# Kernel optimization log

Measured on AMD Instinct MI355X. Metric: run time of the kernel, lower is better.

Reference implementation:

```python
import jax, jax.numpy as jnp
import numpy as np
jax.config.update('jax_enable_x64', True)

T = 524288      # hash table size (2^19)
D = 3           # input_dim
F = 2           # feature_dim
L = 16          # levels
N_MIN, N_MAX = 16, 512
B = 262144      # batch of query points
V = 2 ** D      # voxel corners

_b = np.exp((np.log(N_MAX) - np.log(N_MIN)) / (L - 1))
RESOLUTIONS = jnp.asarray(np.floor(N_MIN * _b ** np.arange(L)).astype(np.int64)).reshape(1, 1, L, 1)
PRIMES = jnp.asarray(np.array([1, 2654435761, 805459861], dtype=np.int64))
_border = np.empty((D, V), dtype=np.int64)
for i in range(D):
    _border[i, :] = np.array(([0] * 2 ** i + [1] * 2 ** i) * 2 ** (D - i - 1), dtype=np.int64)
BORDER_ADDS = jnp.asarray(_border).reshape(1, D, 1, V)


def setup_inputs() -> dict:
    key = jax.random.key(0)
    kx, kt = jax.random.split(key)
    x = jax.random.uniform(kx, (B, D), dtype=jnp.float32)  # coords in [0,1)
    # nn.Embedding init: uniform(-1e-4, 1e-4) per level
    tables = jax.random.uniform(kt, (L, T, F), dtype=jnp.float32, minval=-1e-4, maxval=1e-4)
    return {"x": x, "tables": tables}


def reference(x, tables):
    # scale to each grid resolution: (B, D, L, 1)
    scaled = x[:, :, None, None] * RESOLUTIONS.astype(x.dtype)
    # voxel corner integer coords: (B, D, L, V)
    grid = jnp.floor(scaled).astype(jnp.int64) + BORDER_ADDS
    # NVIDIA fast hash: xor of coord*prime over dims, mod T -> (B, L, V)
    hashed = grid * PRIMES.reshape(1, D, 1, 1)
    idx = jnp.remainder(jnp.bitwise_xor(jnp.bitwise_xor(hashed[:, 0], hashed[:, 1]), hashed[:, 2]), T)
    # gather per-level features: (B, L, V, F)
    feats = tables[jnp.arange(L)[None, :, None], idx]
    # multilinear interpolation weights: prod over dims -> (B, L, V)
    w = jnp.prod(1.0 - jnp.abs(scaled - grid.astype(scaled.dtype)), axis=1)
    # weighted corner sum -> (B, L, F) -> (B, L*F)
    out = jnp.einsum('blv,blvf->blf', w, feats)
    return out.reshape(x.shape[0], L * F)
```

## Files before the change

### kernel.cpp

```cpp
#include <hip/hip_runtime.h>


constexpr int      kT      = 524288;
constexpr unsigned kMask   = kT - 1;
constexpr int      kB      = 262144;
constexpr unsigned kP1     = 2654435761u;
constexpr unsigned kP2     = 805459861u;
constexpr int      kBins   = 4096;
constexpr int      kCap    = 128;
constexpr int      kOvfCap = 65536;
constexpr int      kCoopTot = 845;

typedef float f32x4 __attribute__((ext_vector_type(4)));
typedef float f32x2 __attribute__((ext_vector_type(2)));

__device__ __forceinline__ unsigned morton12(float x0, float x1, float x2) {
    unsigned a = min(15u, (unsigned)(x0 * 16.0f));
    unsigned b = min(15u, (unsigned)(x1 * 16.0f));
    unsigned c = min(15u, (unsigned)(x2 * 16.0f));
    unsigned key = 0;
#pragma unroll
    for (int i = 3; i >= 0; --i)
        key = (key << 3) | (((a >> i) & 1u) << 2) | (((b >> i) & 1u) << 1) | ((c >> i) & 1u);
    return key;
}

__device__ __forceinline__ f32x2 direct_level(const float x0, const float x1, const float x2,
                                              const float res,
                                              const f32x4* __restrict__ tab4) {
    const float s0 = x0 * res, s1 = x1 * res, s2 = x2 * res;
    const float f0 = floorf(s0), f1 = floorf(s1), f2 = floorf(s2);
    const float r0 = s0 - f0, r1 = s1 - f1, r2 = s2 - f2;
    const unsigned c0 = (unsigned)f0;
    const unsigned h1a = (unsigned)f1 * kP1, h1b = h1a + kP1;
    const unsigned h2a = (unsigned)f2 * kP2, h2b = h2a + kP2;
    const float w0a = 1.0f - r0, w1a = 1.0f - r1, w2a = 1.0f - r2;
    float a0 = 0.0f, a1 = 0.0f;
#pragma unroll
    for (int q = 0; q < 4; ++q) {
        const unsigned g = ((q & 1) ? h1b : h1a) ^ ((q & 2) ? h2b : h2a);
        const unsigned i0 = (c0 ^ g) & kMask;
        const unsigned i1 = ((c0 + 1u) ^ g) & kMask;
        const f32x4 A = tab4[i0 >> 1];
        const f32x4 B = tab4[i1 >> 1];
        const float p0x = (i0 & 1) ? A.z : A.x;
        const float p0y = (i0 & 1) ? A.w : A.y;
        const float p1x = (i1 & 1) ? B.z : B.x;
        const float p1y = (i1 & 1) ? B.w : B.y;
        const float wyz = ((q & 1) ? r1 : w1a) * ((q & 2) ? r2 : w2a);
        const float wl = wyz * w0a;
        const float wr = wyz * r0;
        a0 = fmaf(wl, p0x, fmaf(wr, p1x, a0));
        a1 = fmaf(wl, p0y, fmaf(wr, p1y, a1));
    }
    f32x2 r; r.x = a0; r.y = a1;
    return r;
}

__device__ __forceinline__ f32x2 direct_level_masked(const float x0, const float x1, const float x2,
                                                     const float res,
                                                     const f32x4* __restrict__ tab4) {
    const float s0 = x0 * res, s1 = x1 * res, s2 = x2 * res;
    const float f0 = floorf(s0), f1 = floorf(s1), f2 = floorf(s2);
    const float r0 = s0 - f0, r1 = s1 - f1, r2 = s2 - f2;
    const unsigned c0 = (unsigned)f0;
    const unsigned h1a = (unsigned)f1 * kP1, h1b = h1a + kP1;
    const unsigned h2a = (unsigned)f2 * kP2, h2b = h2a + kP2;
    const float w0a = 1.0f - r0, w1a = 1.0f - r1, w2a = 1.0f - r2;

    unsigned i0[4], i1[4];
#pragma unroll
    for (int q = 0; q < 4; ++q) {
        const unsigned g = ((q & 1) ? h1b : h1a) ^ ((q & 2) ? h2b : h2a);
        i0[q] = (c0 ^ g) & kMask;
        i1[q] = ((c0 + 1u) ^ g) & kMask;
    }
    f32x4 A[4];
#pragma unroll
    for (int q = 0; q < 4; ++q) A[q] = tab4[i0[q] >> 1];
    const bool odd = (c0 & 1u) != 0u;
    f32x4 Bv[4];
    if (odd) {
#pragma unroll
        for (int q = 0; q < 4; ++q) Bv[q] = tab4[i1[q] >> 1];
    }
    float a0 = 0.0f, a1 = 0.0f;
#pragma unroll
    for (int q = 0; q < 4; ++q) {
        const float p0x = (i0[q] & 1) ? A[q].z : A[q].x;
        const float p0y = (i0[q] & 1) ? A[q].w : A[q].y;
        const float ex = (i1[q] & 1) ? A[q].z : A[q].x;
        const float ey = (i1[q] & 1) ? A[q].w : A[q].y;
        const float bx_ = (i1[q] & 1) ? Bv[q].z : Bv[q].x;
        const float by_ = (i1[q] & 1) ? Bv[q].w : Bv[q].y;
        const float p1x = odd ? bx_ : ex;
        const float p1y = odd ? by_ : ey;
        const float wyz = ((q & 1) ? r1 : w1a) * ((q & 2) ? r2 : w2a);
        const float wl = wyz * w0a;
        const float wr = wyz * r0;
        a0 = fmaf(wl, p0x, fmaf(wr, p1x, a0));
        a1 = fmaf(wl, p0y, fmaf(wr, p1y, a1));
    }
    f32x2 r; r.x = a0; r.y = a1;
    return r;
}

__device__ __forceinline__ void hashenc_body(const float x0, const float x1, const float x2,
                                             const f32x4* __restrict__ tab4base,
                                             f32x4* __restrict__ out, const unsigned sid) {
    f32x4 o[8];
    constexpr float kResF[16] = {16, 20, 25, 32, 40, 50, 64, 80,
                                 101, 128, 161, 203, 256, 322, 406, 512};
#pragma unroll
    for (int l = 0; l < 16; ++l) {
        const f32x2 r = direct_level(x0, x1, x2, kResF[l], tab4base + (size_t)l * (kT / 2));
        if (l & 1) { o[l >> 1].z = r.x; o[l >> 1].w = r.y; }
        else       { o[l >> 1].x = r.x; o[l >> 1].y = r.y; }
    }
    f32x4* op = out + (size_t)sid * 8;
#pragma unroll
    for (int k = 0; k < 8; ++k) __builtin_nontemporal_store(o[k], op + k);
}

template <int L, int N, int RES, int OFF>
__device__ __forceinline__ void coop_fill(const unsigned lane,
                                          const unsigned bx, const unsigned by, const unsigned bz,
                                          const f32x2* __restrict__ tab2,
                                          f32x2* __restrict__ wlds) {
    const unsigned lo0 = (bx * RES) >> 4, lo1 = (by * RES) >> 4, lo2 = (bz * RES) >> 4;
    const unsigned h1 = lo1 * kP1, h2 = lo2 * kP2;
    constexpr int NC = N * N * N;
#pragma unroll
    for (int k = 0; k < (NC + 63) / 64; ++k) {
        const int t = (int)lane + 64 * k;
        if (t < NC) {
            const unsigned dx = (unsigned)t / (N * N);
            const unsigned rem = (unsigned)t % (N * N);
            const unsigned dy = rem / N, dz = rem % N;
            const unsigned idx = ((lo0 + dx) ^ (h1 + dy * kP1) ^ (h2 + dz * kP2)) & kMask;
            wlds[OFF + t] = tab2[(size_t)L * kT + idx];
        }
    }
}

template <int N, int RES, int OFF>
__device__ __forceinline__ f32x2 coop_interp(const float x0, const float x1, const float x2,
                                             const unsigned bx, const unsigned by, const unsigned bz,
                                             const f32x2* __restrict__ wlds) {
    const float res = (float)RES;
    const float s0 = x0 * res, s1 = x1 * res, s2 = x2 * res;
    const float f0 = floorf(s0), f1 = floorf(s1), f2 = floorf(s2);
    const float r0 = s0 - f0, r1 = s1 - f1, r2 = s2 - f2;
    const unsigned lo0 = (bx * RES) >> 4, lo1 = (by * RES) >> 4, lo2 = (bz * RES) >> 4;
    const unsigned i0 = min((unsigned)f0 - lo0, (unsigned)(N - 2));
    const unsigned i1 = min((unsigned)f1 - lo1, (unsigned)(N - 2));
    const unsigned i2 = min((unsigned)f2 - lo2, (unsigned)(N - 2));
    const int s00 = OFF + (int)(i0 * (N * N) + i1 * N + i2);
    const f32x2 c000 = wlds[s00],             c001 = wlds[s00 + 1];
    const f32x2 c010 = wlds[s00 + N],         c011 = wlds[s00 + N + 1];
    const f32x2 c100 = wlds[s00 + N * N],     c101 = wlds[s00 + N * N + 1];
    const f32x2 c110 = wlds[s00 + N * N + N], c111 = wlds[s00 + N * N + N + 1];
    const float w0a = 1.f - r0, w1a = 1.f - r1, w2a = 1.f - r2;
    const float w00 = w0a * w1a, w01 = w0a * r1, w10 = r0 * w1a, w11 = r0 * r1;
    float a0 = w00 * w2a * c000.x;
    float a1 = w00 * w2a * c000.y;
    a0 = fmaf(w00 * r2,  c001.x, a0); a1 = fmaf(w00 * r2,  c001.y, a1);
    a0 = fmaf(w01 * w2a, c010.x, a0); a1 = fmaf(w01 * w2a, c010.y, a1);
    a0 = fmaf(w01 * r2,  c011.x, a0); a1 = fmaf(w01 * r2,  c011.y, a1);
    a0 = fmaf(w10 * w2a, c100.x, a0); a1 = fmaf(w10 * w2a, c100.y, a1);
    a0 = fmaf(w10 * r2,  c101.x, a0); a1 = fmaf(w10 * r2,  c101.y, a1);
    a0 = fmaf(w11 * w2a, c110.x, a0); a1 = fmaf(w11 * w2a, c110.y, a1);
    a0 = fmaf(w11 * r2,  c111.x, a0); a1 = fmaf(w11 * r2,  c111.y, a1);
    f32x2 r; r.x = a0; r.y = a1;
    return r;
}

__global__ __launch_bounds__(256) void scatter_kernel(const float* __restrict__ x,
                                                      unsigned* __restrict__ cnt,
                                                      f32x4* __restrict__ xsort,
                                                      f32x4* __restrict__ ovf) {
    const int i = blockIdx.x * 256 + threadIdx.x;
    const float x0 = x[3 * i], x1 = x[3 * i + 1], x2 = x[3 * i + 2];
    const unsigned key = morton12(x0, x1, x2);
    const unsigned slot = atomicAdd(&cnt[key], 1u);
    f32x4 v;
    v.x = x0; v.y = x1; v.z = x2; v.w = __uint_as_float((unsigned)i);
    if (slot < (unsigned)kCap) {
        xsort[key * kCap + slot] = v;
    } else {
        const unsigned o = atomicAdd(&cnt[kBins], 1u);
        if (o < (unsigned)kOvfCap) ovf[o] = v;
    }
}

__global__ __launch_bounds__(256, 5) void hashenc_main(const float* __restrict__ x,
                                                       const f32x4* __restrict__ xsort,
                                                       const unsigned* __restrict__ cnt,
                                                       const f32x2* __restrict__ tab2,
                                                       const f32x4* __restrict__ tab4base,
                                                       f32x4* __restrict__ out) {
    __shared__ f32x2 lds[4][kCoopTot];
    const int tid = threadIdx.x;
    const int b = (int)blockIdx.x;

    if (b < 2048) {
        constexpr float kFineRes[8] = {101, 128, 161, 203, 256, 322, 406, 512};
        const int j = b & 7;
        const int chunk = b >> 3;
        const float res = kFineRes[j];
        const f32x4* __restrict__ tab4 = tab4base + (size_t)(8 + j) * (kT / 2);
        f32x2* __restrict__ out2 = (f32x2*)out;
        const int sbase = chunk * 1024 + tid;
#pragma unroll
        for (int it = 0; it < 4; ++it) {
            const int s = sbase + 256 * it;
            const float x0 = x[3 * s + 0];
            const float x1 = x[3 * s + 1];
            const float x2 = x[3 * s + 2];
            const f32x2 r = direct_level_masked(x0, x1, x2, res, tab4);
            __builtin_nontemporal_store(r, out2 + (size_t)s * 16 + 8 + j);
        }
        return;
    }

    const int c = b - 2048;
    const int bid = (int)((c & 7) * 256 + (c >> 3));
    const int gs  = bid * 256 + tid;
    const int bin = gs >> 7;
    const int sl  = gs & (kCap - 1);
    const unsigned n = min(cnt[bin], (unsigned)kCap);
    if ((unsigned)(sl & 64) >= n) return;
    const bool valid = (unsigned)sl < n;
    const f32x4 v = xsort[gs];
    const float x0 = valid ? v.x : 0.5f;
    const float x1 = valid ? v.y : 0.5f;
    const float x2 = valid ? v.z : 0.5f;

    const unsigned key = (unsigned)bin;
    const unsigned bx = ((key >> 2) & 1) | ((key >> 4) & 2) | ((key >> 6) & 4) | ((key >> 8) & 8);
    const unsigned by = ((key >> 1) & 1) | ((key >> 3) & 2) | ((key >> 5) & 4) | ((key >> 7) & 8);
    const unsigned bz = ((key     ) & 1) | ((key >> 2) & 2) | ((key >> 4) & 4) | ((key >> 6) & 8);

    f32x2* wlds = lds[tid >> 6];
    const unsigned lane = (unsigned)(tid & 63);

    coop_fill<0, 2, 16,   0>(lane, bx, by, bz, tab2, wlds);
    coop_fill<1, 4, 20,   8>(lane, bx, by, bz, tab2, wlds);
    coop_fill<2, 4, 25,  72>(lane, bx, by, bz, tab2, wlds);
    coop_fill<3, 3, 32, 136>(lane, bx, by, bz, tab2, wlds);
    coop_fill<4, 5, 40, 163>(lane, bx, by, bz, tab2, wlds);
    coop_fill<5, 6, 50, 288>(lane, bx, by, bz, tab2, wlds);
    coop_fill<6, 5, 64, 504>(lane, bx, by, bz, tab2, wlds);
    coop_fill<7, 6, 80, 629>(lane, bx, by, bz, tab2, wlds);

    f32x4 o0, o1, o2, o3;
    { const f32x2 r = coop_interp<2, 16,   0>(x0, x1, x2, bx, by, bz, wlds); o0.x = r.x; o0.y = r.y; }
    { const f32x2 r = coop_interp<4, 20,   8>(x0, x1, x2, bx, by, bz, wlds); o0.z = r.x; o0.w = r.y; }
    { const f32x2 r = coop_interp<4, 25,  72>(x0, x1, x2, bx, by, bz, wlds); o1.x = r.x; o1.y = r.y; }
    { const f32x2 r = coop_interp<3, 32, 136>(x0, x1, x2, bx, by, bz, wlds); o1.z = r.x; o1.w = r.y; }
    { const f32x2 r = coop_interp<5, 40, 163>(x0, x1, x2, bx, by, bz, wlds); o2.x = r.x; o2.y = r.y; }
    { const f32x2 r = coop_interp<6, 50, 288>(x0, x1, x2, bx, by, bz, wlds); o2.z = r.x; o2.w = r.y; }
    { const f32x2 r = coop_interp<5, 64, 504>(x0, x1, x2, bx, by, bz, wlds); o3.x = r.x; o3.y = r.y; }
    { const f32x2 r = coop_interp<6, 80, 629>(x0, x1, x2, bx, by, bz, wlds); o3.z = r.x; o3.w = r.y; }

    if (valid) {
        f32x4* op = out + (size_t)__float_as_uint(v.w) * 8;
        __builtin_nontemporal_store(o0, op + 0);
        __builtin_nontemporal_store(o1, op + 1);
        __builtin_nontemporal_store(o2, op + 2);
        __builtin_nontemporal_store(o3, op + 3);
    }
}

__global__ __launch_bounds__(256) void cleanup_kernel(const f32x4* __restrict__ ovf,
                                                      const unsigned* __restrict__ cnt,
                                                      const f32x4* __restrict__ tab4base,
                                                      f32x4* __restrict__ out) {
    const unsigned oc = min(cnt[kBins], (unsigned)kOvfCap);
    for (unsigned j = threadIdx.x; j < oc; j += 256) {
        const f32x4 v = ovf[j];
        hashenc_body(v.x, v.y, v.z, tab4base, out, __float_as_uint(v.w));
    }
}

__global__ __launch_bounds__(256, 4) void hashenc_direct(const float* __restrict__ x,
                                                         const f32x4* __restrict__ tab4base,
                                                         f32x4* __restrict__ out) {
    const int i = blockIdx.x * 256 + threadIdx.x;
    hashenc_body(x[3 * i], x[3 * i + 1], x[3 * i + 2], tab4base, out, (unsigned)i);
}

extern "C" void kernel_launch(void* const* d_in, const int* in_sizes, int n_in,
                              void* d_out, int out_size, void* d_ws, size_t ws_size,
                              hipStream_t stream) {
    const float*  x    = (const float*)d_in[0];
    const f32x2*  tab2 = (const f32x2*)d_in[1];
    const f32x4*  tab4 = (const f32x4*)d_in[1];
    f32x4*        out  = (f32x4*)d_out;

    const size_t cntBytes   = (size_t)(kBins + 16) * 4;
    const size_t ovfBytes   = (size_t)kOvfCap * 16;
    const size_t xsortBytes = (size_t)kBins * kCap * 16;
    const size_t need = cntBytes + ovfBytes + xsortBytes;

    if (ws_size >= need) {
        unsigned* cnt   = (unsigned*)d_ws;
        f32x4*    ovf   = (f32x4*)((char*)d_ws + cntBytes);
        f32x4*    xsort = ovf + kOvfCap;
        hipMemsetAsync(cnt, 0, cntBytes, stream);
        scatter_kernel<<<kB / 256, 256, 0, stream>>>(x, cnt, xsort, ovf);
        hashenc_main<<<4096, 256, 0, stream>>>(x, xsort, cnt, tab2, tab4, out);
        cleanup_kernel<<<1, 256, 0, stream>>>(ovf, cnt, tab4, out);
    } else {
        hashenc_direct<<<kB / 256, 256, 0, stream>>>(x, tab4, out);
    }
}
```

Before: 132.1 us.

## Share per-bin coarse-level LDS tiles across two wavefronts per bin

Each 128-point bin now fills its coarse-level LDS neighbourhood using both wavefronts that belong to it, not one tile per wavefront. That halves LDS use per block and the redundant global gathers for the coarse levels. It adds a block-wide __syncthreads and removes the early exit for empty half-bins, so idle wavefronts still take part in the fill. The occupancy hint rises from 5 to 6 blocks per CU to match the smaller LDS footprint.

```diff
diff --git a/kernel.cpp b/kernel.cpp
--- a/kernel.cpp
+++ b/kernel.cpp
@@ -123,22 +123,22 @@
 }
 
 template <int L, int N, int RES, int OFF>
-__device__ __forceinline__ void coop_fill(const unsigned lane,
-                                          const unsigned bx, const unsigned by, const unsigned bz,
-                                          const f32x2* __restrict__ tab2,
-                                          f32x2* __restrict__ wlds) {
+__device__ __forceinline__ void coop_fill128(const unsigned t,
+                                             const unsigned bx, const unsigned by, const unsigned bz,
+                                             const f32x2* __restrict__ tab2,
+                                             f32x2* __restrict__ wlds) {
     const unsigned lo0 = (bx * RES) >> 4, lo1 = (by * RES) >> 4, lo2 = (bz * RES) >> 4;
     const unsigned h1 = lo1 * kP1, h2 = lo2 * kP2;
     constexpr int NC = N * N * N;
 #pragma unroll
-    for (int k = 0; k < (NC + 63) / 64; ++k) {
-        const int t = (int)lane + 64 * k;
-        if (t < NC) {
-            const unsigned dx = (unsigned)t / (N * N);
-            const unsigned rem = (unsigned)t % (N * N);
+    for (int k = 0; k < (NC + 127) / 128; ++k) {
+        const int e = (int)t + 128 * k;
+        if (e < NC) {
+            const unsigned dx = (unsigned)e / (N * N);
+            const unsigned rem = (unsigned)e % (N * N);
             const unsigned dy = rem / N, dz = rem % N;
             const unsigned idx = ((lo0 + dx) ^ (h1 + dy * kP1) ^ (h2 + dz * kP2)) & kMask;
-            wlds[OFF + t] = tab2[(size_t)L * kT + idx];
+            wlds[OFF + e] = tab2[(size_t)L * kT + idx];
         }
     }
 }
@@ -193,13 +193,13 @@
     }
 }
 
-__global__ __launch_bounds__(256, 5) void hashenc_main(const float* __restrict__ x,
+__global__ __launch_bounds__(256, 6) void hashenc_main(const float* __restrict__ x,
                                                        const f32x4* __restrict__ xsort,
                                                        const unsigned* __restrict__ cnt,
                                                        const f32x2* __restrict__ tab2,
                                                        const f32x4* __restrict__ tab4base,
                                                        f32x4* __restrict__ out) {
-    __shared__ f32x2 lds[4][kCoopTot];
+    __shared__ f32x2 lds[2][kCoopTot];
     const int tid = threadIdx.x;
     const int b = (int)blockIdx.x;
 
@@ -229,41 +229,40 @@
     const int bin = gs >> 7;
     const int sl  = gs & (kCap - 1);
     const unsigned n = min(cnt[bin], (unsigned)kCap);
-    if ((unsigned)(sl & 64) >= n) return;
     const bool valid = (unsigned)sl < n;
     const f32x4 v = xsort[gs];
-    const float x0 = valid ? v.x : 0.5f;
-    const float x1 = valid ? v.y : 0.5f;
-    const float x2 = valid ? v.z : 0.5f;
 
     const unsigned key = (unsigned)bin;
     const unsigned bx = ((key >> 2) & 1) | ((key >> 4) & 2) | ((key >> 6) & 4) | ((key >> 8) & 8);
     const unsigned by = ((key >> 1) & 1) | ((key >> 3) & 2) | ((key >> 5) & 4) | ((key >> 7) & 8);
     const unsigned bz = ((key     ) & 1) | ((key >> 2) & 2) | ((key >> 4) & 4) | ((key >> 6) & 8);
 
-    f32x2* wlds = lds[tid >> 6];
-    const unsigned lane = (unsigned)(tid & 63);
-
-    coop_fill<0, 2, 16,   0>(lane, bx, by, bz, tab2, wlds);
-    coop_fill<1, 4, 20,   8>(lane, bx, by, bz, tab2, wlds);
-    coop_fill<2, 4, 25,  72>(lane, bx, by, bz, tab2, wlds);
-    coop_fill<3, 3, 32, 136>(lane, bx, by, bz, tab2, wlds);
-    coop_fill<4, 5, 40, 163>(lane, bx, by, bz, tab2, wlds);
-    coop_fill<5, 6, 50, 288>(lane, bx, by, bz, tab2, wlds);
-    coop_fill<6, 5, 64, 504>(lane, bx, by, bz, tab2, wlds);
-    coop_fill<7, 6, 80, 629>(lane, bx, by, bz, tab2, wlds);
-
-    f32x4 o0, o1, o2, o3;
-    { const f32x2 r = coop_interp<2, 16,   0>(x0, x1, x2, bx, by, bz, wlds); o0.x = r.x; o0.y = r.y; }
-    { const f32x2 r = coop_interp<4, 20,   8>(x0, x1, x2, bx, by, bz, wlds); o0.z = r.x; o0.w = r.y; }
-    { const f32x2 r = coop_interp<4, 25,  72>(x0, x1, x2, bx, by, bz, wlds); o1.x = r.x; o1.y = r.y; }
-    { const f32x2 r = coop_interp<3, 32, 136>(x0, x1, x2, bx, by, bz, wlds); o1.z = r.x; o1.w = r.y; }
-    { const f32x2 r = coop_interp<5, 40, 163>(x0, x1, x2, bx, by, bz, wlds); o2.x = r.x; o2.y = r.y; }
-    { const f32x2 r = coop_interp<6, 50, 288>(x0, x1, x2, bx, by, bz, wlds); o2.z = r.x; o2.w = r.y; }
-    { const f32x2 r = coop_interp<5, 64, 504>(x0, x1, x2, bx, by, bz, wlds); o3.x = r.x; o3.y = r.y; }
-    { const f32x2 r = coop_interp<6, 80, 629>(x0, x1, x2, bx, by, bz, wlds); o3.z = r.x; o3.w = r.y; }
+    f32x2* wlds = lds[tid >> 7];
+    const unsigned t = (unsigned)(tid & 127);
+
+    coop_fill128<0, 2, 16,   0>(t, bx, by, bz, tab2, wlds);
+    coop_fill128<1, 4, 20,   8>(t, bx, by, bz, tab2, wlds);
+    coop_fill128<2, 4, 25,  72>(t, bx, by, bz, tab2, wlds);
+    coop_fill128<3, 3, 32, 136>(t, bx, by, bz, tab2, wlds);
+    coop_fill128<4, 5, 40, 163>(t, bx, by, bz, tab2, wlds);
+    coop_fill128<5, 6, 50, 288>(t, bx, by, bz, tab2, wlds);
+    coop_fill128<6, 5, 64, 504>(t, bx, by, bz, tab2, wlds);
+    coop_fill128<7, 6, 80, 629>(t, bx, by, bz, tab2, wlds);
+
+    __syncthreads();
 
     if (valid) {
+        const float x0 = v.x, x1 = v.y, x2 = v.z;
+        f32x4 o0, o1, o2, o3;
+        { const f32x2 r = coop_interp<2, 16,   0>(x0, x1, x2, bx, by, bz, wlds); o0.x = r.x; o0.y = r.y; }
+        { const f32x2 r = coop_interp<4, 20,   8>(x0, x1, x2, bx, by, bz, wlds); o0.z = r.x; o0.w = r.y; }
+        { const f32x2 r = coop_interp<4, 25,  72>(x0, x1, x2, bx, by, bz, wlds); o1.x = r.x; o1.y = r.y; }
+        { const f32x2 r = coop_interp<3, 32, 136>(x0, x1, x2, bx, by, bz, wlds); o1.z = r.x; o1.w = r.y; }
+        { const f32x2 r = coop_interp<5, 40, 163>(x0, x1, x2, bx, by, bz, wlds); o2.x = r.x; o2.y = r.y; }
+        { const f32x2 r = coop_interp<6, 50, 288>(x0, x1, x2, bx, by, bz, wlds); o2.z = r.x; o2.w = r.y; }
+        { const f32x2 r = coop_interp<5, 64, 504>(x0, x1, x2, bx, by, bz, wlds); o3.x = r.x; o3.y = r.y; }
+        { const f32x2 r = coop_interp<6, 80, 629>(x0, x1, x2, bx, by, bz, wlds); o3.z = r.x; o3.w = r.y; }
+
         f32x4* op = out + (size_t)__float_as_uint(v.w) * 8;
         __builtin_nontemporal_store(o0, op + 0);
         __builtin_nontemporal_store(o1, op + 1);
```

Result: no change. 134.5 us (+1.8%).
